# Performance work log

Measured on AMD Instinct MI355X. Metric: run time of the kernel, lower is better.

## Reference

```python
import jax, jax.numpy as jnp
import numpy as np
import math

B, S, D, H = 2, 2048, 1024, 16
HD = D // H  # head dim = 64


def setup_inputs() -> dict:
    key = jax.random.key(0)
    ks = jax.random.split(key, 8)
    scale = 1.0 / math.sqrt(D)
    return {
        "x": jax.random.normal(ks[0], (B, S, D), dtype=jnp.float32),
        "mask": jax.random.randint(ks[1], (B, S, S), 0, 2).astype(bool),
        "Wq": jax.random.normal(ks[2], (D, D), dtype=jnp.float32) * scale,
        "bq": jax.random.normal(ks[3], (D,), dtype=jnp.float32) * 0.01,
        "Wk": jax.random.normal(ks[4], (D, D), dtype=jnp.float32) * scale,
        "bk": jax.random.normal(ks[5], (D,), dtype=jnp.float32) * 0.01,
        "Wv": jax.random.normal(ks[6], (D, D), dtype=jnp.float32) * scale,
        "bv": jax.random.normal(ks[7], (D,), dtype=jnp.float32) * 0.01,
    }


def reference(x, mask, Wq, bq, Wk, bk, Wv, bv):
    # Linear projections (weights stored as [in, out])
    q = x @ Wq + bq  # [B,S,D]
    k = x @ Wk + bk
    v = x @ Wv + bv
    # split heads -> [B,H,S,HD]
    q = q.reshape(B, S, H, HD).transpose(0, 2, 1, 3)
    k = k.reshape(B, S, H, HD).transpose(0, 2, 1, 3)
    v = v.reshape(B, S, H, HD).transpose(0, 2, 1, 3)
    scores = jnp.einsum("bhqd,bhkd->bhqk", q, k) / jnp.sqrt(jnp.float32(HD))
    # Faithful to the source: masked_fill_(mask, -inf) is immediately
    # overwritten by masked_fill_(mask, 0), so masked positions end up 0
    # BEFORE the softmax (a quirk of the original module).
    scores = jnp.where(mask[:, None, :, :], 0.0, scores)
    attn = jax.nn.softmax(scores, axis=-1)  # dropout=0.0 (eval)
    out = jnp.einsum("bhqk,bhkd->bhqd", attn, v)
    return out.transpose(0, 2, 1, 3).reshape(B, S, D)
```

## Files before the change

kernel.cpp:

```cpp
#include <hip/hip_runtime.h>
#include <cstdint>
#include <cstddef>

static constexpr int B_ = 2, S_ = 2048, D_ = 1024, H_ = 16, HD_ = 64;

typedef float f32x4 __attribute__((ext_vector_type(4)));
typedef short bf16x8 __attribute__((ext_vector_type(8)));

__device__ __forceinline__ unsigned short f2bf(float f) {
    union { float f; unsigned int u; } v; v.f = f;
    unsigned int r = v.u + 0x7FFFu + ((v.u >> 16) & 1u);
    return (unsigned short)(r >> 16);
}

__device__ __forceinline__ unsigned pack2bf(float a, float b) {
    union { float f; unsigned u; } va, vb; va.f = a; vb.f = b;
    unsigned ra = va.u + 0x7FFFu + ((va.u >> 16) & 1u);
    unsigned rb = vb.u + 0x7FFFu + ((vb.u >> 16) & 1u);
    return __builtin_amdgcn_perm(rb, ra, 0x07060302u);
}

__device__ __forceinline__ void gload_lds16(const void* g, void* l) {
    __builtin_amdgcn_global_load_lds(
        (const __attribute__((address_space(1))) void*)g,
        (__attribute__((address_space(3))) void*)l, 16, 0, 0);
}

__global__ __launch_bounds__(256)
void prep(const float* __restrict__ x, unsigned short* __restrict__ xo,
          const int* __restrict__ m, unsigned char* __restrict__ mo,
          const float* __restrict__ Wq, const float* __restrict__ Wk,
          const float* __restrict__ Wv, unsigned short* __restrict__ wt) {
    __shared__ unsigned short Ts[64][72];
    const int bid = blockIdx.x, t = threadIdx.x;
    if (bid < 2048) {
        size_t i = ((size_t)bid * 256 + t) * 8;
        float4 a = *(const float4*)(x + i);
        float4 c = *(const float4*)(x + i + 4);
        uint4 r;
        r.x = pack2bf(a.x, a.y); r.y = pack2bf(a.z, a.w);
        r.z = pack2bf(c.x, c.y); r.w = pack2bf(c.z, c.w);
        *(uint4*)(xo + i) = r;
    } else if (bid < 4096) {
        size_t i = ((size_t)(bid - 2048) * 256 + t) * 16;
        uint4 r;
        unsigned w[4];
        #pragma unroll
        for (int g = 0; g < 4; ++g) {
            int4 v = *(const int4*)(m + i + g * 4);
            w[g] = (v.x ? 0xFFu : 0u) | (v.y ? 0xFF00u : 0u) |
                   (v.z ? 0xFF0000u : 0u) | (v.w ? 0xFF000000u : 0u);
        }
        r.x = w[0]; r.y = w[1]; r.z = w[2]; r.w = w[3];
        *(uint4*)(mo + i) = r;
    } else {
        const int tid = bid - 4096;
        const int mat = tid >> 8, tile = tid & 255;
        const float* __restrict__ W = (mat == 0) ? Wq : (mat == 1) ? Wk : Wv;
        unsigned short* __restrict__ o = wt + (size_t)mat * D_ * D_;
        const int n0 = (tile & 15) * 64, k0 = (tile >> 4) * 64;
        {
            const int nl = t & 63, kb = t >> 6;
            #pragma unroll
            for (int i = 0; i < 16; ++i) {
                int k = kb + i * 4;
                Ts[nl][k] = f2bf(W[(size_t)(k0 + k) * D_ + n0 + nl]);
            }
        }
        __syncthreads();
        {
            const int kl = t & 63, nb = t >> 6;
            #pragma unroll
            for (int i = 0; i < 16; ++i) {
                int n = nb + i * 4;
                o[(size_t)(n0 + n) * D_ + k0 + kl] = Ts[n][kl];
            }
        }
    }
}

__global__ __launch_bounds__(512)
void qkv_gemm(const unsigned short* __restrict__ xb, const unsigned short* __restrict__ wt,
              const float* __restrict__ bq, const float* __restrict__ bk,
              const float* __restrict__ bv,
              unsigned short* __restrict__ qo, unsigned short* __restrict__ ko,
              unsigned short* __restrict__ vto) {
    const int bx = blockIdx.x;
    const int by = blockIdx.y;
    const int mat = bx >> 3;
    const int ncol0 = (bx & 7) * 128;
    const float* __restrict__ bias = (mat == 0) ? bq : (mat == 1) ? bk : bv;
    const unsigned short* __restrict__ Wm = wt + (size_t)mat * D_ * D_;

    __shared__ unsigned short As[2][128 * 32];
    __shared__ unsigned short Bs[2][128 * 32];

    const int t = threadIdx.x;
    const int w = t >> 6, lane = t & 63;
    const int l15 = lane & 15, quad = lane >> 4;
    const int mw = (w >> 2) * 64, nw = (w & 3) * 32;
    const int rowBase = by * 128;

    const int r16 = lane >> 2;
    const int sslot = lane & 3;
    const int sg = (sslot ^ ((r16 >> 1) & 3)) * 8;
    const int srow = w * 16 + r16;
    const int rcol = (quad ^ ((l15 >> 1) & 3)) * 8;

    f32x4 acc[4][2] = {};

    gload_lds16(xb + (size_t)(rowBase + srow) * D_ + sg, &As[0][w * 16 * 32]);
    gload_lds16(Wm + (size_t)(ncol0 + srow) * D_ + sg, &Bs[0][w * 16 * 32]);

    for (int it = 0; it < 32; ++it) {
        const int cur = it & 1;
        __syncthreads();
        if (it + 1 < 32) {
            const int ktn = (it + 1) * 32;
            gload_lds16(xb + (size_t)(rowBase + srow) * D_ + ktn + sg,
                        &As[cur ^ 1][w * 16 * 32]);
            gload_lds16(Wm + (size_t)(ncol0 + srow) * D_ + ktn + sg,
                        &Bs[cur ^ 1][w * 16 * 32]);
        }

        bf16x8 a[4], b[2];
        #pragma unroll
        for (int i = 0; i < 4; ++i)
            a[i] = *(const bf16x8*)&As[cur][(mw + i * 16 + l15) * 32 + rcol];
        #pragma unroll
        for (int j = 0; j < 2; ++j)
            b[j] = *(const bf16x8*)&Bs[cur][(nw + j * 16 + l15) * 32 + rcol];
        #pragma unroll
        for (int i = 0; i < 4; ++i)
            #pragma unroll
            for (int j = 0; j < 2; ++j)
                acc[i][j] = __builtin_amdgcn_mfma_f32_16x16x32_bf16(a[i], b[j], acc[i][j], 0, 0, 0);
    }

    if (mat < 2) {
        unsigned short* __restrict__ O = (mat == 0) ? qo : ko;
        const float osc = (mat == 0) ? 0.18033688011112443f : 1.0f;
        #pragma unroll
        for (int j = 0; j < 2; ++j) {
            const int col = ncol0 + nw + j * 16 + l15;
            const float bb = bias[col];
            #pragma unroll
            for (int i = 0; i < 4; ++i)
                #pragma unroll
                for (int r = 0; r < 4; ++r) {
                    const int m = rowBase + mw + i * 16 + quad * 4 + r;
                    O[(size_t)m * D_ + col] = f2bf((acc[i][j][r] + bb) * osc);
                }
        }
    } else {
        #pragma unroll
        for (int j = 0; j < 2; ++j) {
            const int col = ncol0 + nw + j * 16 + l15;
            const float bb = bias[col];
            const int hh = col >> 6, hd = col & 63;
            #pragma unroll
            for (int i = 0; i < 4; ++i) {
                const int m0 = rowBase + mw + i * 16 + quad * 4;
                const int bg = m0 >> 11, s0 = m0 & 2047;
                ushort4 pk;
                pk.x = f2bf(acc[i][j][0] + bb);
                pk.y = f2bf(acc[i][j][1] + bb);
                pk.z = f2bf(acc[i][j][2] + bb);
                pk.w = f2bf(acc[i][j][3] + bb);
                *(ushort4*)&vto[(((size_t)bg * H_ + hh) * HD_ + hd) * S_ + s0] = pk;
            }
        }
    }
}

__global__ __launch_bounds__(512, 4)
void attn_mfma(const unsigned short* __restrict__ qmat,
               const unsigned short* __restrict__ kmat,
               const unsigned short* __restrict__ vtg,
               const unsigned char* __restrict__ msk, float* __restrict__ out) {
    const int h = blockIdx.x, qt = blockIdx.y, b = blockIdx.z;
    const int t = threadIdx.x, w = t >> 6, lane = t & 63;
    const int l15 = lane & 15, quad = lane >> 4;
    const int q0 = qt * 128;

    __shared__ __align__(16) char smem[49152];
    unsigned short* const Ksm = (unsigned short*)smem;
    unsigned short* const Vsm = (unsigned short*)(smem + 16384);
    unsigned short* const Psm = (unsigned short*)(smem + 32768);

    const size_t bh = (size_t)b * S_ * D_ + (size_t)h * HD_;
    const unsigned short* __restrict__ qp = qmat + bh;
    const unsigned short* __restrict__ kp = kmat + bh;
    const unsigned short* __restrict__ vp = vtg + ((size_t)b * H_ + h) * HD_ * S_;
    const unsigned char* __restrict__ mb = msk + (size_t)b * S_ * S_;

    const int rs = lane >> 3, sslot = lane & 7;
    const int sg = (sslot ^ rs) * 8;
    const int srow = w * 8 + rs;

    const int qs = w >> 1;
    const int kw = (w & 1) * 32;
    const int kst = w & 1;
    const int sw7 = l15 & 7;

    bf16x8 qfr[2][2];
    #pragma unroll
    for (int nt = 0; nt < 2; ++nt)
        #pragma unroll
        for (int dk = 0; dk < 2; ++dk)
            qfr[nt][dk] = *(const bf16x8*)(qp +
                (size_t)(q0 + qs * 32 + nt * 16 + l15) * D_ + dk * 32 + quad * 8);

    f32x4 accO[2][4] = {};
    f32x4 lsA[2] = {};
    bf16x8 ones;
    #pragma unroll
    for (int i = 0; i < 8; ++i) ones[i] = (short)0x3F80;

    gload_lds16(kp + (size_t)srow * D_ + sg, Ksm + w * 8 * 64);
    gload_lds16(vp + (size_t)srow * S_ + sg, Vsm + w * 8 * 64);

    for (int it = 0; it < 32; ++it) {
        const int cur = it & 1;
        const int kt = it * 64;
        __syncthreads();

        unsigned mu[2][2];
        #pragma unroll
        for (int nt = 0; nt < 2; ++nt) {
            const unsigned char* __restrict__ mrow =
                mb + (size_t)(q0 + qs * 32 + nt * 16 + l15) * S_ + kt + kw;
            mu[nt][0] = *(const unsigned*)(mrow + quad * 4);
            mu[nt][1] = *(const unsigned*)(mrow + 16 + quad * 4);
        }

        if (it + 1 < 32) {
            const int ktn = kt + 64;
            gload_lds16(kp + (size_t)(ktn + srow) * D_ + sg,
                        Ksm + (cur ^ 1) * 4096 + w * 8 * 64);
            gload_lds16(vp + (size_t)srow * S_ + ktn + sg,
                        Vsm + (cur ^ 1) * 4096 + w * 8 * 64);
        }

        f32x4 sc[2][2] = {};
        #pragma unroll
        for (int dk = 0; dk < 2; ++dk) {
            bf16x8 kfr[2];
            #pragma unroll
            for (int mt = 0; mt < 2; ++mt) {
                const int R = kw + mt * 16 + l15;
                kfr[mt] = *(const bf16x8*)&Ksm[cur * 4096 + R * 64 +
                                               (((dk * 4 + quad) ^ sw7) * 8)];
            }
            __builtin_amdgcn_s_setprio(1);
            #pragma unroll
            for (int nt = 0; nt < 2; ++nt)
                #pragma unroll
                for (int mt = 0; mt < 2; ++mt)
                    sc[nt][mt] = __builtin_amdgcn_mfma_f32_16x16x32_bf16(
                        kfr[mt], qfr[nt][dk], sc[nt][mt], 0, 0, 0);
            __builtin_amdgcn_s_setprio(0);
        }

        #pragma unroll
        for (int nt = 0; nt < 2; ++nt) {
            const int qr = qs * 32 + nt * 16 + l15;
            #pragma unroll
            for (int mt = 0; mt < 2; ++mt) {
                const int mtg = kst * 2 + mt;
                unsigned p0 = pack2bf(__builtin_amdgcn_exp2f(sc[nt][mt][0]),
                                      __builtin_amdgcn_exp2f(sc[nt][mt][1]));
                unsigned p1 = pack2bf(__builtin_amdgcn_exp2f(sc[nt][mt][2]),
                                      __builtin_amdgcn_exp2f(sc[nt][mt][3]));
                const unsigned m0 = __builtin_amdgcn_perm(0u, mu[nt][mt], 0x01010000u);
                const unsigned m1 = __builtin_amdgcn_perm(0u, mu[nt][mt], 0x03030202u);
                p0 = (m0 & 0x3F803F80u) | (~m0 & p0);
                p1 = (m1 & 0x3F803F80u) | (~m1 & p1);
                uint2 pk2; pk2.x = p0; pk2.y = p1;
                *(uint2*)((char*)Psm + qr * 128 +
                          (((2 * mtg + (quad >> 1)) ^ sw7) * 16) + (quad & 1) * 8) = pk2;
            }
        }

        {
            bf16x8 vfr[4];
            #pragma unroll
            for (int dt = 0; dt < 4; ++dt) {
                const int R = dt * 16 + l15;
                vfr[dt] = *(const bf16x8*)&Vsm[cur * 4096 + R * 64 +
                                               (((kst * 4 + quad) ^ sw7) * 8)];
            }
            #pragma unroll
            for (int nt = 0; nt < 2; ++nt) {
                const int qr = qs * 32 + nt * 16 + l15;
                bf16x8 pfr = *(const bf16x8*)((const char*)Psm + qr * 128 +
                                              (((kst * 4 + quad) ^ sw7) * 16));
                __builtin_amdgcn_s_setprio(1);
                #pragma unroll
                for (int dt = 0; dt < 4; ++dt)
                    accO[nt][dt] = __builtin_amdgcn_mfma_f32_16x16x32_bf16(
                        pfr, vfr[dt], accO[nt][dt], 0, 0, 0);
                lsA[nt] = __builtin_amdgcn_mfma_f32_16x16x32_bf16(pfr, ones, lsA[nt], 0, 0, 0);
                __builtin_amdgcn_s_setprio(0);
            }
        }
    }

    __syncthreads();
    float* const Red = (float*)smem;
    if (w & 1) {
        #pragma unroll
        for (int nt = 0; nt < 2; ++nt) {
            const int pidx = ((qs * 2 + nt) * 64 + lane) * 20;
            #pragma unroll
            for (int dt = 0; dt < 4; ++dt)
                *(f32x4*)&Red[pidx + dt * 4] = accO[nt][dt];
            *(f32x4*)&Red[pidx + 16] = lsA[nt];
        }
    }
    __syncthreads();
    if (!(w & 1)) {
        float* __restrict__ ob = out + ((size_t)b * S_ + q0) * D_ + (size_t)h * HD_;
        #pragma unroll
        for (int nt = 0; nt < 2; ++nt) {
            const int pidx = ((qs * 2 + nt) * 64 + lane) * 20;
            #pragma unroll
            for (int dt = 0; dt < 4; ++dt)
                accO[nt][dt] += *(const f32x4*)&Red[pidx + dt * 4];
            lsA[nt] += *(const f32x4*)&Red[pidx + 16];

            #pragma unroll
            for (int r = 0; r < 4; ++r) {
                const float inv = 1.0f / lsA[nt][r];
                const int row = qs * 32 + nt * 16 + quad * 4 + r;
                #pragma unroll
                for (int dt = 0; dt < 4; ++dt)
                    ob[(size_t)row * D_ + dt * 16 + l15] = accO[nt][dt][r] * inv;
            }
        }
    }
}

extern "C" void kernel_launch(void* const* d_in, const int* in_sizes, int n_in,
                              void* d_out, int out_size, void* d_ws, size_t ws_size,
                              hipStream_t stream) {
    (void)in_sizes; (void)n_in; (void)out_size; (void)ws_size;
    const float* x    = (const float*)d_in[0];
    const int*   mask = (const int*)d_in[1];
    const float* Wq   = (const float*)d_in[2];
    const float* bq   = (const float*)d_in[3];
    const float* Wk   = (const float*)d_in[4];
    const float* bk   = (const float*)d_in[5];
    const float* Wv   = (const float*)d_in[6];
    const float* bv   = (const float*)d_in[7];
    float* out = (float*)d_out;

    const size_t M1 = (size_t)1024 * 1024;
    unsigned short* xb  = (unsigned short*)d_ws;
    unsigned short* wtb = xb + 4 * M1;
    unsigned short* qb  = wtb + 3 * M1;
    unsigned short* kb  = qb + 4 * M1;
    unsigned short* vtb = kb + 4 * M1;
    unsigned char*  mk  = (unsigned char*)(vtb + 4 * M1);

    prep<<<4864, 256, 0, stream>>>(x, xb, mask, mk, Wq, Wk, Wv, wtb);
    qkv_gemm<<<dim3(24, 32), 512, 0, stream>>>(xb, wtb, bq, bk, bv, qb, kb, vtb);
    attn_mfma<<<dim3(16, 16, 2), 512, 0, stream>>>(qb, kb, vtb, mk, out);
}
```

Before: 210.3 us.

## Split attention key range across two blocks and add reduction kernel

The attention kernel now splits the 2048-key range into two halves, each handled by a separate block, which doubles the grid from 512 to 1024 blocks. Each half writes unnormalised partial outputs and row sums to workspace, and a new reduce kernel adds them and divides by the summed denominator. The main loop is manually unrolled by two so the double-buffer index is a compile-time constant, and launch bounds are raised to 6 blocks per SM. The extra parallelism is meant to fill the GPU better, at the cost of about 32 MB of extra fp32 partial traffic and an additional kernel launch.

```diff
diff --git a/kernel.cpp b/kernel.cpp
--- a/kernel.cpp
+++ b/kernel.cpp
@@ -173,12 +173,14 @@
     }
 }
 
-__global__ __launch_bounds__(512, 4)
+__global__ __launch_bounds__(512, 6)
 void attn_mfma(const unsigned short* __restrict__ qmat,
                const unsigned short* __restrict__ kmat,
                const unsigned short* __restrict__ vtg,
-               const unsigned char* __restrict__ msk, float* __restrict__ out) {
-    const int h = blockIdx.x, qt = blockIdx.y, b = blockIdx.z;
+               const unsigned char* __restrict__ msk,
+               float* __restrict__ opart, float* __restrict__ lspart) {
+    const int h = blockIdx.x, yy = blockIdx.y, b = blockIdx.z;
+    const int qt = yy >> 1, half = yy & 1;
     const int t = threadIdx.x, w = t >> 6, lane = t & 63;
     const int l15 = lane & 15, quad = lane >> 4;
     const int q0 = qt * 128;
@@ -190,9 +192,9 @@
 
     const size_t bh = (size_t)b * S_ * D_ + (size_t)h * HD_;
     const unsigned short* __restrict__ qp = qmat + bh;
-    const unsigned short* __restrict__ kp = kmat + bh;
-    const unsigned short* __restrict__ vp = vtg + ((size_t)b * H_ + h) * HD_ * S_;
-    const unsigned char* __restrict__ mb = msk + (size_t)b * S_ * S_;
+    const unsigned short* __restrict__ kp = kmat + bh + (size_t)half * 1024 * D_;
+    const unsigned short* __restrict__ vp = vtg + ((size_t)b * H_ + h) * HD_ * S_ + half * 1024;
+    const unsigned char* __restrict__ mb = msk + (size_t)b * S_ * S_ + half * 1024;
 
     const int rs = lane >> 3, sslot = lane & 7;
     const int sg = (sslot ^ rs) * 8;
@@ -220,91 +222,96 @@
     gload_lds16(kp + (size_t)srow * D_ + sg, Ksm + w * 8 * 64);
     gload_lds16(vp + (size_t)srow * S_ + sg, Vsm + w * 8 * 64);
 
-    for (int it = 0; it < 32; ++it) {
-        const int cur = it & 1;
-        const int kt = it * 64;
-        __syncthreads();
-
-        unsigned mu[2][2];
-        #pragma unroll
-        for (int nt = 0; nt < 2; ++nt) {
-            const unsigned char* __restrict__ mrow =
-                mb + (size_t)(q0 + qs * 32 + nt * 16 + l15) * S_ + kt + kw;
-            mu[nt][0] = *(const unsigned*)(mrow + quad * 4);
-            mu[nt][1] = *(const unsigned*)(mrow + 16 + quad * 4);
-        }
-
-        if (it + 1 < 32) {
-            const int ktn = kt + 64;
-            gload_lds16(kp + (size_t)(ktn + srow) * D_ + sg,
-                        Ksm + (cur ^ 1) * 4096 + w * 8 * 64);
-            gload_lds16(vp + (size_t)srow * S_ + ktn + sg,
-                        Vsm + (cur ^ 1) * 4096 + w * 8 * 64);
-        }
-
-        f32x4 sc[2][2] = {};
-        #pragma unroll
-        for (int dk = 0; dk < 2; ++dk) {
-            bf16x8 kfr[2];
-            #pragma unroll
-            for (int mt = 0; mt < 2; ++mt) {
-                const int R = kw + mt * 16 + l15;
-                kfr[mt] = *(const bf16x8*)&Ksm[cur * 4096 + R * 64 +
-                                               (((dk * 4 + quad) ^ sw7) * 8)];
-            }
-            __builtin_amdgcn_s_setprio(1);
-            #pragma unroll
-            for (int nt = 0; nt < 2; ++nt)
-                #pragma unroll
-                for (int mt = 0; mt < 2; ++mt)
-                    sc[nt][mt] = __builtin_amdgcn_mfma_f32_16x16x32_bf16(
-                        kfr[mt], qfr[nt][dk], sc[nt][mt], 0, 0, 0);
-            __builtin_amdgcn_s_setprio(0);
-        }
-
-        #pragma unroll
-        for (int nt = 0; nt < 2; ++nt) {
-            const int qr = qs * 32 + nt * 16 + l15;
-            #pragma unroll
-            for (int mt = 0; mt < 2; ++mt) {
-                const int mtg = kst * 2 + mt;
-                unsigned p0 = pack2bf(__builtin_amdgcn_exp2f(sc[nt][mt][0]),
-                                      __builtin_amdgcn_exp2f(sc[nt][mt][1]));
-                unsigned p1 = pack2bf(__builtin_amdgcn_exp2f(sc[nt][mt][2]),
-                                      __builtin_amdgcn_exp2f(sc[nt][mt][3]));
-                const unsigned m0 = __builtin_amdgcn_perm(0u, mu[nt][mt], 0x01010000u);
-                const unsigned m1 = __builtin_amdgcn_perm(0u, mu[nt][mt], 0x03030202u);
-                p0 = (m0 & 0x3F803F80u) | (~m0 & p0);
-                p1 = (m1 & 0x3F803F80u) | (~m1 & p1);
-                uint2 pk2; pk2.x = p0; pk2.y = p1;
-                *(uint2*)((char*)Psm + qr * 128 +
-                          (((2 * mtg + (quad >> 1)) ^ sw7) * 16) + (quad & 1) * 8) = pk2;
-            }
-        }
-
-        {
-            bf16x8 vfr[4];
-            #pragma unroll
-            for (int dt = 0; dt < 4; ++dt) {
-                const int R = dt * 16 + l15;
-                vfr[dt] = *(const bf16x8*)&Vsm[cur * 4096 + R * 64 +
-                                               (((kst * 4 + quad) ^ sw7) * 8)];
-            }
-            #pragma unroll
-            for (int nt = 0; nt < 2; ++nt) {
-                const int qr = qs * 32 + nt * 16 + l15;
-                bf16x8 pfr = *(const bf16x8*)((const char*)Psm + qr * 128 +
-                                              (((kst * 4 + quad) ^ sw7) * 16));
-                __builtin_amdgcn_s_setprio(1);
-                #pragma unroll
-                for (int dt = 0; dt < 4; ++dt)
-                    accO[nt][dt] = __builtin_amdgcn_mfma_f32_16x16x32_bf16(
-                        pfr, vfr[dt], accO[nt][dt], 0, 0, 0);
-                lsA[nt] = __builtin_amdgcn_mfma_f32_16x16x32_bf16(pfr, ones, lsA[nt], 0, 0, 0);
-                __builtin_amdgcn_s_setprio(0);
-            }
-        }
-    }
+#define ATTN_STEP(IT, CUR)                                                     \
+    do {                                                                       \
+        const int kt = (IT) * 64;                                              \
+        __syncthreads();                                                       \
+        unsigned mu[2][2];                                                     \
+        _Pragma("unroll")                                                      \
+        for (int nt = 0; nt < 2; ++nt) {                                       \
+            const unsigned char* __restrict__ mrow =                           \
+                mb + (size_t)(q0 + qs * 32 + nt * 16 + l15) * S_ + kt + kw;    \
+            mu[nt][0] = *(const unsigned*)(mrow + quad * 4);                   \
+            mu[nt][1] = *(const unsigned*)(mrow + 16 + quad * 4);              \
+        }                                                                      \
+        if ((IT) + 1 < 16) {                                                   \
+            const int ktn = kt + 64;                                           \
+            gload_lds16(kp + (size_t)(ktn + srow) * D_ + sg,                   \
+                        Ksm + ((CUR) ^ 1) * 4096 + w * 8 * 64);                \
+            gload_lds16(vp + (size_t)srow * S_ + ktn + sg,                     \
+                        Vsm + ((CUR) ^ 1) * 4096 + w * 8 * 64);                \
+        }                                                                      \
+        f32x4 sc[2][2] = {};                                                   \
+        _Pragma("unroll")                                                      \
+        for (int dk = 0; dk < 2; ++dk) {                                       \
+            bf16x8 kfr[2];                                                     \
+            _Pragma("unroll")                                                  \
+            for (int mt = 0; mt < 2; ++mt) {                                   \
+                const int R = kw + mt * 16 + l15;                              \
+                kfr[mt] = *(const bf16x8*)&Ksm[(CUR) * 4096 + R * 64 +         \
+                                               (((dk * 4 + quad) ^ sw7) * 8)]; \
+            }                                                                  \
+            __builtin_amdgcn_s_setprio(1);                                     \
+            _Pragma("unroll")                                                  \
+            for (int nt = 0; nt < 2; ++nt)                                     \
+                _Pragma("unroll")                                              \
+                for (int mt = 0; mt < 2; ++mt)                                 \
+                    sc[nt][mt] = __builtin_amdgcn_mfma_f32_16x16x32_bf16(      \
+                        kfr[mt], qfr[nt][dk], sc[nt][mt], 0, 0, 0);            \
+            __builtin_amdgcn_s_setprio(0);                                     \
+        }                                                                      \
+        _Pragma("unroll")                                                      \
+        for (int nt = 0; nt < 2; ++nt) {                                       \
+            const int qr = qs * 32 + nt * 16 + l15;                            \
+            _Pragma("unroll")                                                  \
+            for (int mt = 0; mt < 2; ++mt) {                                   \
+                const int mtg = kst * 2 + mt;                                  \
+                unsigned p0 = pack2bf(__builtin_amdgcn_exp2f(sc[nt][mt][0]),   \
+                                      __builtin_amdgcn_exp2f(sc[nt][mt][1]));  \
+                unsigned p1 = pack2bf(__builtin_amdgcn_exp2f(sc[nt][mt][2]),   \
+                                      __builtin_amdgcn_exp2f(sc[nt][mt][3]));  \
+                const unsigned m0 =                                            \
+                    __builtin_amdgcn_perm(0u, mu[nt][mt], 0x01010000u);        \
+                const unsigned m1 =                                            \
+                    __builtin_amdgcn_perm(0u, mu[nt][mt], 0x03030202u);        \
+                p0 = (m0 & 0x3F803F80u) | (~m0 & p0);                          \
+                p1 = (m1 & 0x3F803F80u) | (~m1 & p1);                          \
+                uint2 pk2; pk2.x = p0; pk2.y = p1;                             \
+                *(uint2*)((char*)Psm + qr * 128 +                              \
+                          (((2 * mtg + (quad >> 1)) ^ sw7) * 16) +             \
+                          (quad & 1) * 8) = pk2;                               \
+            }                                                                  \
+        }                                                                      \
+        {                                                                      \
+            bf16x8 vfr[4];                                                     \
+            _Pragma("unroll")                                                  \
+            for (int dt = 0; dt < 4; ++dt) {                                   \
+                const int R = dt * 16 + l15;                                   \
+                vfr[dt] = *(const bf16x8*)&Vsm[(CUR) * 4096 + R * 64 +         \
+                                               (((kst * 4 + quad) ^ sw7) * 8)];\
+            }                                                                  \
+            _Pragma("unroll")                                                  \
+            for (int nt = 0; nt < 2; ++nt) {                                   \
+                const int qr = qs * 32 + nt * 16 + l15;                        \
+                bf16x8 pfr = *(const bf16x8*)((const char*)Psm + qr * 128 +    \
+                                              (((kst * 4 + quad) ^ sw7) * 16));\
+                __builtin_amdgcn_s_setprio(1);                                 \
+                _Pragma("unroll")                                              \
+                for (int dt = 0; dt < 4; ++dt)                                 \
+                    accO[nt][dt] = __builtin_amdgcn_mfma_f32_16x16x32_bf16(    \
+                        pfr, vfr[dt], accO[nt][dt], 0, 0, 0);                  \
+                lsA[nt] = __builtin_amdgcn_mfma_f32_16x16x32_bf16(             \
+                    pfr, ones, lsA[nt], 0, 0, 0);                              \
+                __builtin_amdgcn_s_setprio(0);                                 \
+            }                                                                  \
+        }                                                                      \
+    } while (0)
+
+    for (int io = 0; io < 8; ++io) {
+        ATTN_STEP(2 * io, 0);
+        ATTN_STEP(2 * io + 1, 1);
+    }
+#undef ATTN_STEP
 
     __syncthreads();
     float* const Red = (float*)smem;
@@ -320,7 +327,8 @@
     }
     __syncthreads();
     if (!(w & 1)) {
-        float* __restrict__ ob = out + ((size_t)b * S_ + q0) * D_ + (size_t)h * HD_;
+        float* __restrict__ op = opart +
+            (((size_t)half * B_ + b) * S_ + q0) * D_ + (size_t)h * HD_;
         #pragma unroll
         for (int nt = 0; nt < 2; ++nt) {
             const int pidx = ((qs * 2 + nt) * 64 + lane) * 20;
@@ -331,14 +339,42 @@
 
             #pragma unroll
             for (int r = 0; r < 4; ++r) {
-                const float inv = 1.0f / lsA[nt][r];
                 const int row = qs * 32 + nt * 16 + quad * 4 + r;
                 #pragma unroll
                 for (int dt = 0; dt < 4; ++dt)
-                    ob[(size_t)row * D_ + dt * 16 + l15] = accO[nt][dt][r] * inv;
+                    op[(size_t)row * D_ + dt * 16 + l15] = accO[nt][dt][r];
             }
-        }
-    }
+            if (l15 == 0) {
+                #pragma unroll
+                for (int r = 0; r < 4; ++r) {
+                    const int row = qs * 32 + nt * 16 + quad * 4 + r;
+                    lspart[(((size_t)half * B_ + b) * H_ + h) * S_ + q0 + row] =
+                        lsA[nt][r];
+                }
+            }
+        }
+    }
+}
+
+__global__ __launch_bounds__(256)
+void attn_reduce(const float* __restrict__ Op, const float* __restrict__ Ls,
+                 float* __restrict__ out) {
+    const size_t i = ((size_t)blockIdx.x * 256 + threadIdx.x) * 4;
+    const size_t HALF = (size_t)B_ * S_ * D_;
+    float4 p0 = *(const float4*)(Op + i);
+    float4 p1 = *(const float4*)(Op + HALF + i);
+    const int rowg = (int)(i >> 10);
+    const int col = (int)(i & 1023);
+    const int b = rowg >> 11, row = rowg & 2047, h = col >> 6;
+    const float l = Ls[((size_t)b * H_ + h) * S_ + row] +
+                    Ls[((size_t)(B_ + b) * H_ + h) * S_ + row];
+    const float inv = 1.0f / l;
+    float4 o;
+    o.x = (p0.x + p1.x) * inv;
+    o.y = (p0.y + p1.y) * inv;
+    o.z = (p0.z + p1.z) * inv;
+    o.w = (p0.w + p1.w) * inv;
+    *(float4*)(out + i) = o;
 }
 
 extern "C" void kernel_launch(void* const* d_in, const int* in_sizes, int n_in,
@@ -362,8 +398,11 @@
     unsigned short* kb  = qb + 4 * M1;
     unsigned short* vtb = kb + 4 * M1;
     unsigned char*  mk  = (unsigned char*)(vtb + 4 * M1);
+    float* opart = (float*)(mk + 8 * M1);
+    float* lspart = opart + 2 * (size_t)B_ * S_ * D_;
 
     prep<<<4864, 256, 0, stream>>>(x, xb, mask, mk, Wq, Wk, Wv, wtb);
     qkv_gemm<<<dim3(24, 32), 512, 0, stream>>>(xb, wtb, bq, bk, bv, qb, kb, vtb);
-    attn_mfma<<<dim3(16, 16, 2), 512, 0, stream>>>(qb, kb, vtb, mk, out);
-}
+    attn_mfma<<<dim3(16, 32, 2), 512, 0, stream>>>(qb, kb, vtb, mk, opart, lspart);
+    attn_reduce<<<4096, 256, 0, stream>>>(opart, lspart, out);
+}
```

After: 518.0 us. 2.46x slower.

## Software-pipeline PV matmul one iteration behind QK with double-buffered P

Applied to the files above, without the earlier changes.

Restructures the attention main loop so the P·V MFMAs for the previous key tile are issued right after the current tile's Q·K MFMAs, before the exp/mask/P-store stage. The P scratch buffer is double-buffered and V is triple-buffered in LDS, and a drain step after the loop handles the last tile. The aim is to hide the softmax-exponent and LDS write latency behind independent matrix work. In exchange, LDS per block grows from 48 KB to 72 KB, which can lower the number of resident blocks per CU.

```diff
diff --git a/kernel.cpp b/kernel.cpp
--- a/kernel.cpp
+++ b/kernel.cpp
@@ -183,10 +183,10 @@
     const int l15 = lane & 15, quad = lane >> 4;
     const int q0 = qt * 128;
 
-    __shared__ __align__(16) char smem[49152];
+    __shared__ __align__(16) char smem[73728];
     unsigned short* const Ksm = (unsigned short*)smem;
     unsigned short* const Vsm = (unsigned short*)(smem + 16384);
-    unsigned short* const Psm = (unsigned short*)(smem + 32768);
+    char* const Psm = smem + 40960;
 
     const size_t bh = (size_t)b * S_ * D_ + (size_t)h * HD_;
     const unsigned short* __restrict__ qp = qmat + bh;
@@ -220,6 +220,8 @@
     gload_lds16(kp + (size_t)srow * D_ + sg, Ksm + w * 8 * 64);
     gload_lds16(vp + (size_t)srow * S_ + sg, Vsm + w * 8 * 64);
 
+    int v_im1 = 2, v_i = 0, v_ip1 = 1;
+
     for (int it = 0; it < 32; ++it) {
         const int cur = it & 1;
         const int kt = it * 64;
@@ -239,7 +241,7 @@
             gload_lds16(kp + (size_t)(ktn + srow) * D_ + sg,
                         Ksm + (cur ^ 1) * 4096 + w * 8 * 64);
             gload_lds16(vp + (size_t)srow * S_ + ktn + sg,
-                        Vsm + (cur ^ 1) * 4096 + w * 8 * 64);
+                        Vsm + v_ip1 * 4096 + w * 8 * 64);
         }
 
         f32x4 sc[2][2] = {};
@@ -260,6 +262,29 @@
                     sc[nt][mt] = __builtin_amdgcn_mfma_f32_16x16x32_bf16(
                         kfr[mt], qfr[nt][dk], sc[nt][mt], 0, 0, 0);
             __builtin_amdgcn_s_setprio(0);
+        }
+
+        if (it > 0) {
+            bf16x8 vfr[4];
+            #pragma unroll
+            for (int dt = 0; dt < 4; ++dt) {
+                const int R = dt * 16 + l15;
+                vfr[dt] = *(const bf16x8*)&Vsm[v_im1 * 4096 + R * 64 +
+                                               (((kst * 4 + quad) ^ sw7) * 8)];
+            }
+            #pragma unroll
+            for (int nt = 0; nt < 2; ++nt) {
+                const int qr = qs * 32 + nt * 16 + l15;
+                bf16x8 pfr = *(const bf16x8*)(Psm + (cur ^ 1) * 16384 + qr * 128 +
+                                              (((kst * 4 + quad) ^ sw7) * 16));
+                __builtin_amdgcn_s_setprio(1);
+                #pragma unroll
+                for (int dt = 0; dt < 4; ++dt)
+                    accO[nt][dt] = __builtin_amdgcn_mfma_f32_16x16x32_bf16(
+                        pfr, vfr[dt], accO[nt][dt], 0, 0, 0);
+                lsA[nt] = __builtin_amdgcn_mfma_f32_16x16x32_bf16(pfr, ones, lsA[nt], 0, 0, 0);
+                __builtin_amdgcn_s_setprio(0);
+            }
         }
 
         #pragma unroll
@@ -277,32 +302,32 @@
                 p0 = (m0 & 0x3F803F80u) | (~m0 & p0);
                 p1 = (m1 & 0x3F803F80u) | (~m1 & p1);
                 uint2 pk2; pk2.x = p0; pk2.y = p1;
-                *(uint2*)((char*)Psm + qr * 128 +
+                *(uint2*)(Psm + cur * 16384 + qr * 128 +
                           (((2 * mtg + (quad >> 1)) ^ sw7) * 16) + (quad & 1) * 8) = pk2;
             }
         }
 
-        {
-            bf16x8 vfr[4];
-            #pragma unroll
-            for (int dt = 0; dt < 4; ++dt) {
-                const int R = dt * 16 + l15;
-                vfr[dt] = *(const bf16x8*)&Vsm[cur * 4096 + R * 64 +
-                                               (((kst * 4 + quad) ^ sw7) * 8)];
-            }
-            #pragma unroll
-            for (int nt = 0; nt < 2; ++nt) {
-                const int qr = qs * 32 + nt * 16 + l15;
-                bf16x8 pfr = *(const bf16x8*)((const char*)Psm + qr * 128 +
-                                              (((kst * 4 + quad) ^ sw7) * 16));
-                __builtin_amdgcn_s_setprio(1);
-                #pragma unroll
-                for (int dt = 0; dt < 4; ++dt)
-                    accO[nt][dt] = __builtin_amdgcn_mfma_f32_16x16x32_bf16(
-                        pfr, vfr[dt], accO[nt][dt], 0, 0, 0);
-                lsA[nt] = __builtin_amdgcn_mfma_f32_16x16x32_bf16(pfr, ones, lsA[nt], 0, 0, 0);
-                __builtin_amdgcn_s_setprio(0);
-            }
+        const int tmpv = v_im1; v_im1 = v_i; v_i = v_ip1; v_ip1 = tmpv;
+    }
+
+    {
+        bf16x8 vfr[4];
+        #pragma unroll
+        for (int dt = 0; dt < 4; ++dt) {
+            const int R = dt * 16 + l15;
+            vfr[dt] = *(const bf16x8*)&Vsm[v_im1 * 4096 + R * 64 +
+                                           (((kst * 4 + quad) ^ sw7) * 8)];
+        }
+        #pragma unroll
+        for (int nt = 0; nt < 2; ++nt) {
+            const int qr = qs * 32 + nt * 16 + l15;
+            bf16x8 pfr = *(const bf16x8*)(Psm + 16384 + qr * 128 +
+                                          (((kst * 4 + quad) ^ sw7) * 16));
+            #pragma unroll
+            for (int dt = 0; dt < 4; ++dt)
+                accO[nt][dt] = __builtin_amdgcn_mfma_f32_16x16x32_bf16(
+                    pfr, vfr[dt], accO[nt][dt], 0, 0, 0);
+            lsA[nt] = __builtin_amdgcn_mfma_f32_16x16x32_bf16(pfr, ones, lsA[nt], 0, 0, 0);
         }
     }
 
```

Result: no change. 214.4 us (+1.9%).
